# Kernel optimization log

Measured on AMD Instinct MI355X. Metric: run time of the kernel, lower is better.

The kernel has to match this reference:

```python
import jax, jax.numpy as jnp
import numpy as np

N0, N1, N2 = 1200000, 120000, 12000  # nodes per hop (outermost -> seeds)
E0, E1 = 1200000, 120000
IN_C, HID_C, OUT_C = 256, 256, 64


def setup_inputs() -> dict:
    key = jax.random.key(0)
    ks = jax.random.split(key, 10)
    s_in, s_hid = 1.0 / np.sqrt(IN_C), 1.0 / np.sqrt(HID_C)
    return {
        "x": jax.random.normal(ks[0], (N0, IN_C), dtype=jnp.float32),
        "src0": jax.random.randint(ks[1], (E0,), 0, N0, dtype=jnp.int64),
        "dst0": jax.random.randint(ks[2], (E0,), 0, N1, dtype=jnp.int64),
        "src1": jax.random.randint(ks[3], (E1,), 0, N1, dtype=jnp.int64),
        "dst1": jax.random.randint(ks[4], (E1,), 0, N2, dtype=jnp.int64),
        "Wl0": jax.random.normal(ks[5], (HID_C, IN_C), dtype=jnp.float32) * s_in,
        "b0": jnp.zeros((HID_C,), dtype=jnp.float32),
        "Wr0": jax.random.normal(ks[6], (HID_C, IN_C), dtype=jnp.float32) * s_in,
        "Wl1": jax.random.normal(ks[7], (OUT_C, HID_C), dtype=jnp.float32) * s_hid,
        "b1": jnp.zeros((OUT_C,), dtype=jnp.float32),
        "Wr1": jax.random.normal(ks[8], (OUT_C, HID_C), dtype=jnp.float32) * s_hid,
    }


def _sage_conv(x_src, x_tgt, src, dst, Wl, b, Wr, n_tgt):
    # gather neighbor (source) features, mean-scatter onto targets
    msg = x_src[src]                                          # [E, C]
    agg = jax.ops.segment_sum(msg, dst, num_segments=n_tgt)   # [n_tgt, C]
    cnt = jax.ops.segment_sum(jnp.ones((dst.shape[0],), x_src.dtype), dst,
                              num_segments=n_tgt)
    agg = agg / jnp.maximum(cnt, 1.0)[:, None]
    return agg @ Wl.T + b + x_tgt @ Wr.T


def reference(x, src0, dst0, src1, dst1, Wl0, b0, Wr0, Wl1, b1, Wr1):
    # layer 0 (eval mode: dropout is identity)
    h = _sage_conv(x, x[:N1], src0, dst0, Wl0, b0, Wr0, N1)
    h = jax.nn.relu(h)
    # layer 1
    out = _sage_conv(h, h[:N2], src1, dst1, Wl1, b1, Wr1, N2)
    return jax.nn.log_softmax(out, axis=-1)
```

## Files before the change

### kernel.cpp

```cpp
#include <hip/hip_runtime.h>
#include <stdint.h>

#define N0c 1200000
#define N1c 120000
#define N2c 12000
#define E0c 1200000
#define E1c 120000
#define NB0 118
#define NB1 12
#define N1pad 120064
#define N2pad 12032
#define ROWB 80
#define ROWU 40
#define HB 5157
#define WCB 768

typedef short short8 __attribute__((ext_vector_type(8)));
typedef float f32x4 __attribute__((ext_vector_type(4)));
typedef unsigned short u16;

__device__ __forceinline__ u16 f2bf(float f) {
    union { float f; unsigned u; } v; v.f = f;
    unsigned r = v.u + 0x7FFFu + ((v.u >> 16) & 1u);
    return (u16)(r >> 16);
}

__device__ __forceinline__ void gload16(const char* g, char* l) {
    __builtin_amdgcn_global_load_lds(
        (const __attribute__((address_space(1))) void*)g,
        (__attribute__((address_space(3))) void*)l, 16, 0, 0);
}

__global__ void k_hist(const int* __restrict__ dst0, const int* __restrict__ dst1,
                       int* __restrict__ c0, int* __restrict__ c1,
                       u16* __restrict__ Bt0, const float* __restrict__ Wl0,
                       const float* __restrict__ Wr0, u16* __restrict__ Bt1,
                       const float* __restrict__ Wl1, const float* __restrict__ Wr1) {
    if (blockIdx.x < HB) {
        int i = blockIdx.x * 256 + threadIdx.x;
        int part = blockIdx.x & 7;
        if (i < E0c) atomicAdd(&c0[part * N1c + dst0[i]], 1);
        else if (i < E0c + E1c) atomicAdd(&c1[part * N2c + dst1[i - E0c]], 1);
    } else {
        int i = (blockIdx.x - HB) * 256 + threadIdx.x;
        if (i < 256 * 512) {
            int c = i >> 9, k = i & 511;
            float v = (k < 256) ? Wl0[c * 256 + k] : Wr0[c * 256 + (k - 256)];
            Bt0[((size_t)(k >> 5) * 256 + c) * ROWU + (k & 31)] = f2bf(v);
        } else {
            int j = i - 256 * 512;
            int c = j >> 9, k = j & 511;
            float v = 0.f;
            if (c < 64) v = (k < 256) ? Wl1[c * 256 + k] : Wr1[c * 256 + (k - 256)];
            Bt1[j] = f2bf(v);
        }
    }
}

__global__ void k_scanA(const int* __restrict__ c0, const int* __restrict__ c1,
                        int* __restrict__ partials) {
    __shared__ int sh[256];
    int hop = blockIdx.x >= NB0;
    int blk = hop ? blockIdx.x - NB0 : blockIdx.x;
    const int* c = hop ? c1 : c0;
    int n = hop ? N2c : N1c;
    int d0 = blk * 1024 + threadIdx.x * 4;
    int tsum = 0;
#pragma unroll
    for (int j = 0; j < 4; ++j) {
        int d = d0 + j;
        if (d < n)
#pragma unroll
            for (int k = 0; k < 8; ++k) tsum += c[k * n + d];
    }
    sh[threadIdx.x] = tsum;
    __syncthreads();
    for (int ofs = 128; ofs > 0; ofs >>= 1) {
        if (threadIdx.x < ofs) sh[threadIdx.x] += sh[threadIdx.x + ofs];
        __syncthreads();
    }
    if (threadIdx.x == 0) partials[blockIdx.x] = sh[0];
}

__global__ void k_scanB(int* __restrict__ partials, int* __restrict__ rs0,
                        int* __restrict__ rs1) {
    __shared__ int sh[256];
    int tid = threadIdx.x;
    int v0 = tid < NB0 ? partials[tid] : 0;
    sh[tid] = v0; __syncthreads();
    for (int ofs = 1; ofs < 256; ofs <<= 1) {
        int t = tid >= ofs ? sh[tid - ofs] : 0;
        __syncthreads();
        sh[tid] += t;
        __syncthreads();
    }
    if (tid < NB0) partials[tid] = sh[tid] - v0;
    __syncthreads();
    int v1 = tid < NB1 ? partials[NB0 + tid] : 0;
    sh[tid] = v1; __syncthreads();
    for (int ofs = 1; ofs < 256; ofs <<= 1) {
        int t = tid >= ofs ? sh[tid - ofs] : 0;
        __syncthreads();
        sh[tid] += t;
        __syncthreads();
    }
    if (tid < NB1) partials[NB0 + tid] = sh[tid] - v1;
    if (tid == 0) { rs0[N1c] = E0c; rs1[N2c] = E1c; }
}

__global__ void k_scanC(const int* __restrict__ c0, const int* __restrict__ c1,
                        const int* __restrict__ partials, int* __restrict__ rs0,
                        int* __restrict__ rs1, int* __restrict__ bs0,
                        int* __restrict__ bs1) {
    __shared__ int sh[256];
    int hop = blockIdx.x >= NB0;
    int blk = hop ? blockIdx.x - NB0 : blockIdx.x;
    const int* c = hop ? c1 : c0;
    int* rs = hop ? rs1 : rs0;
    int* bs = hop ? bs1 : bs0;
    int n = hop ? N2c : N1c;
    int tid = threadIdx.x;
    int d0 = blk * 1024 + tid * 4;
    int cv[4][8];
    int tsum = 0;
#pragma unroll
    for (int j = 0; j < 4; ++j)
#pragma unroll
        for (int k = 0; k < 8; ++k) {
            int d = d0 + j;
            int v = (d < n) ? c[k * n + d] : 0;
            cv[j][k] = v; tsum += v;
        }
    sh[tid] = tsum; __syncthreads();
    for (int ofs = 1; ofs < 256; ofs <<= 1) {
        int t = tid >= ofs ? sh[tid - ofs] : 0;
        __syncthreads();
        sh[tid] += t;
        __syncthreads();
    }
    int run = partials[blockIdx.x] + sh[tid] - tsum;
#pragma unroll
    for (int j = 0; j < 4; ++j) {
        int d = d0 + j;
        if (d < n) {
            rs[d] = run;
#pragma unroll
            for (int k = 0; k < 8; ++k) { bs[k * n + d] = run; run += cv[j][k]; }
        }
    }
}

__global__ void k_scat(const int* __restrict__ src0, const int* __restrict__ dst0,
                       const int* __restrict__ src1, const int* __restrict__ dst1,
                       int* __restrict__ c0, int* __restrict__ c1,
                       const int* __restrict__ bs0, const int* __restrict__ bs1,
                       int* __restrict__ eidx0, int* __restrict__ eidx1) {
    int i = blockIdx.x * 256 + threadIdx.x;
    int part = blockIdx.x & 7;
    if (i < E0c) {
        int d = dst0[i];
        int off = atomicSub(&c0[part * N1c + d], 1) - 1;
        eidx0[bs0[part * N1c + d] + off] = src0[i];
    } else if (i < E0c + E1c) {
        int j = i - E0c;
        int d = dst1[j];
        int off = atomicSub(&c1[part * N2c + d], 1) - 1;
        eidx1[bs1[part * N2c + d] + off] = src1[j];
    }
}

__global__ void k_agg0(const float* __restrict__ x, const int* __restrict__ eidx,
                       const int* __restrict__ rs, u16* __restrict__ A, int ntgt) {
    int w = (int)((blockIdx.x * blockDim.x + threadIdx.x) >> 6);
    int lane = threadIdx.x & 63;
    if (w >= ntgt) return;
    int s = rs[w], e = rs[w + 1];
    float a0 = 0.f, a1 = 0.f, a2 = 0.f, a3 = 0.f;
    int i = s;
    for (; i + 8 <= e; i += 8) {
        f32x4 v[8];
#pragma unroll
        for (int u = 0; u < 8; ++u)
            v[u] = __builtin_nontemporal_load(
                ((const f32x4*)(x + (long)eidx[i + u] * 256)) + lane);
#pragma unroll
        for (int u = 0; u < 8; ++u) {
            a0 += v[u][0]; a1 += v[u][1]; a2 += v[u][2]; a3 += v[u][3];
        }
    }
    for (; i + 2 <= e; i += 2) {
        f32x4 v0 = __builtin_nontemporal_load(
            ((const f32x4*)(x + (long)eidx[i] * 256)) + lane);
        f32x4 v1 = __builtin_nontemporal_load(
            ((const f32x4*)(x + (long)eidx[i + 1] * 256)) + lane);
        a0 += v0[0] + v1[0]; a1 += v0[1] + v1[1];
        a2 += v0[2] + v1[2]; a3 += v0[3] + v1[3];
    }
    if (i < e) {
        f32x4 v = __builtin_nontemporal_load(
            ((const f32x4*)(x + (long)eidx[i] * 256)) + lane);
        a0 += v[0]; a1 += v[1]; a2 += v[2]; a3 += v[3];
    }
    int c = e - s; if (c < 1) c = 1;
    float sc = 1.f / (float)c;
    int kt = lane >> 3;
    int cu = (lane & 7) * 4;
    ushort4 oa;
    oa.x = f2bf(a0 * sc); oa.y = f2bf(a1 * sc); oa.z = f2bf(a2 * sc); oa.w = f2bf(a3 * sc);
    *(ushort4*)(A + ((size_t)kt * N1pad + w) * ROWU + cu) = oa;
}

__global__ void k_agg1(const u16* __restrict__ hsrc, const int* __restrict__ eidx,
                       const int* __restrict__ rs, u16* __restrict__ A, int ntgt) {
    int w = (int)((blockIdx.x * blockDim.x + threadIdx.x) >> 6);
    int lane = threadIdx.x & 63;
    if (w >= ntgt) return;
    int s = rs[w], e = rs[w + 1];
    float a0 = 0.f, a1 = 0.f, a2 = 0.f, a3 = 0.f;
    auto acc4 = [&](ushort4 v) {
        union { unsigned u; float f; } c0, c1, c2, c3;
        c0.u = (unsigned)v.x << 16; c1.u = (unsigned)v.y << 16;
        c2.u = (unsigned)v.z << 16; c3.u = (unsigned)v.w << 16;
        a0 += c0.f; a1 += c1.f; a2 += c2.f; a3 += c3.f;
    };
    int i = s;
    for (; i + 4 <= e; i += 4) {
        ushort4 v0 = ((const ushort4*)(hsrc + (long)eidx[i] * 256))[lane];
        ushort4 v1 = ((const ushort4*)(hsrc + (long)eidx[i + 1] * 256))[lane];
        ushort4 v2 = ((const ushort4*)(hsrc + (long)eidx[i + 2] * 256))[lane];
        ushort4 v3 = ((const ushort4*)(hsrc + (long)eidx[i + 3] * 256))[lane];
        acc4(v0); acc4(v1); acc4(v2); acc4(v3);
    }
    for (; i < e; ++i) {
        ushort4 v = ((const ushort4*)(hsrc + (long)eidx[i] * 256))[lane];
        acc4(v);
    }
    int c = e - s; if (c < 1) c = 1;
    float sc = 1.f / (float)c;
    ushort4 o;
    o.x = f2bf(a0 * sc); o.y = f2bf(a1 * sc); o.z = f2bf(a2 * sc); o.w = f2bf(a3 * sc);
    *(ushort4*)(A + (long)w * 512 + lane * 4) = o;
    ushort4 sv = ((const ushort4*)(hsrc + (long)w * 256))[lane];
    *(ushort4*)(A + (long)w * 512 + 256 + lane * 4) = sv;
}

__global__ __launch_bounds__(512)
void k_gemm0(const u16* __restrict__ A0, const float* __restrict__ x,
             const u16* __restrict__ Bt, const float* __restrict__ bias,
             u16* __restrict__ outp) {
    __shared__ int4 Lbuf[2 * 30720 / 16];
    char* L = (char*)Lbuf;
    const int tid = threadIdx.x;
    const int lane = tid & 63, wid = tid >> 6;
    const int wm = wid >> 2, wn = wid & 3;
    const long m0 = (long)blockIdx.x * 128;

    f32x4 acc[4][4];
#pragma unroll
    for (int i = 0; i < 4; ++i)
#pragma unroll
        for (int j = 0; j < 4; ++j) acc[i][j] = (f32x4){0.f, 0.f, 0.f, 0.f};

    const char* Abase = (const char*)A0 + m0 * ROWB;
    const char* Bbase = (const char*)Bt;
    const int srow = tid >> 2, scq = tid & 3;

    auto stage = [&](int buf, int kt) {
        char* lb = L + buf * 30720;
        const char* gb = Bbase + (size_t)kt * (256 * ROWB);
        if (kt < 8) {
            const char* ga = Abase + (size_t)kt * ((size_t)N1pad * ROWB);
#pragma unroll
            for (int c0 = 0; c0 < 4; ++c0) {
                int c = wid + c0 * 8;
                if (c < 30) {
                    const char* g = (c < 10) ? (ga + c * 1024) : (gb + (c - 10) * 1024);
                    gload16(g + lane * 16, lb + c * 1024);
                }
            }
        } else {
#pragma unroll
            for (int c0 = 0; c0 < 3; ++c0) {
                int c = wid + c0 * 8;
                if (c < 20) gload16(gb + c * 1024 + lane * 16, lb + 10240 + c * 1024);
            }
            const f32x4* p =
                (const f32x4*)(x + (m0 + srow) * 256 + (kt - 8) * 32 + scq * 8);
            f32x4 v0 = p[0], v1 = p[1];
            ushort4 h0, h1;
            h0.x = f2bf(v0[0]); h0.y = f2bf(v0[1]); h0.z = f2bf(v0[2]); h0.w = f2bf(v0[3]);
            h1.x = f2bf(v1[0]); h1.y = f2bf(v1[1]); h1.z = f2bf(v1[2]); h1.w = f2bf(v1[3]);
            ushort4* d = (ushort4*)(lb + srow * ROWB + scq * 16);
            d[0] = h0; d[1] = h1;
        }
    };

    stage(0, 0);
    const int rr = lane & 15, gg = lane >> 4;
    for (int ks = 0; ks < 16; ++ks) {
        int cur = ks & 1;
        __syncthreads();
        if (ks + 1 < 16) stage(cur ^ 1, ks + 1);
        const char* lb = L + cur * 30720;
        short8 af[4], bv[4];
#pragma unroll
        for (int f = 0; f < 4; ++f) {
            af[f] = *(const short8*)(lb + (wm * 64 + f * 16 + rr) * ROWB + gg * 16);
            bv[f] = *(const short8*)(lb + 10240 + (wn * 64 + f * 16 + rr) * ROWB + gg * 16);
        }
#pragma unroll
        for (int i = 0; i < 4; ++i)
#pragma unroll
            for (int j = 0; j < 4; ++j)
                acc[i][j] =
                    __builtin_amdgcn_mfma_f32_16x16x32_bf16(af[i], bv[j], acc[i][j], 0, 0, 0);
    }

#pragma unroll
    for (int j = 0; j < 4; ++j) {
        int col = wn * 64 + j * 16 + rr;
        float bvl = bias[col];
#pragma unroll
        for (int i = 0; i < 4; ++i) {
            long row = m0 + wm * 64 + i * 16 + gg * 4;
#pragma unroll
            for (int q = 0; q < 4; ++q) {
                long r = row + q;
                if (r < N1c) {
                    float v = acc[i][j][q] + bvl;
                    v = v > 0.f ? v : 0.f;
                    outp[r * 256 + col] = f2bf(v);
                }
            }
        }
    }
}

__global__ __launch_bounds__(256)
void k_gemm1(const u16* __restrict__ A, const u16* __restrict__ Bt,
             const float* __restrict__ bias, float* __restrict__ outp) {
    __shared__ u16 As[128 * 40];
    __shared__ u16 Bs[128 * 40];
    const int tid = threadIdx.x;
    const int lane = tid & 63, wid = tid >> 6;
    const int wm = wid >> 1, wn = wid & 1;
    const long m0 = (long)blockIdx.x * 128;
    const int sar = tid >> 1, sac = (tid & 1) * 16;

    f32x4 acc[4][4];
#pragma unroll
    for (int i = 0; i < 4; ++i)
#pragma unroll
        for (int j = 0; j < 4; ++j) acc[i][j] = (f32x4){0.f, 0.f, 0.f, 0.f};

    int4 ra[2]; int4 rb[2];
    auto load_tile = [&](int ks) {
        int k0 = ks * 32;
        const int4* p = (const int4*)(A + (m0 + sar) * 512 + k0 + sac);
        ra[0] = p[0]; ra[1] = p[1];
        const int4* q = (const int4*)(Bt + (long)sar * 512 + k0 + sac);
        rb[0] = q[0]; rb[1] = q[1];
    };
    auto write_tile = [&]() {
        int4* da = (int4*)(As + sar * 40 + sac);
        da[0] = ra[0]; da[1] = ra[1];
        int4* db = (int4*)(Bs + sar * 40 + sac);
        db[0] = rb[0]; db[1] = rb[1];
    };

    load_tile(0);
    for (int ks = 0; ks < 16; ++ks) {
        __syncthreads();
        write_tile();
        __syncthreads();
        if (ks + 1 < 16) load_tile(ks + 1);
        short8 af[4], bv[4];
        const int rr = lane & 15, gg = lane >> 4;
#pragma unroll
        for (int f = 0; f < 4; ++f) {
            af[f] = *(const short8*)(As + (wm * 64 + f * 16 + rr) * 40 + gg * 8);
            bv[f] = *(const short8*)(Bs + (wn * 64 + f * 16 + rr) * 40 + gg * 8);
        }
#pragma unroll
        for (int i = 0; i < 4; ++i)
#pragma unroll
            for (int j = 0; j < 4; ++j)
                acc[i][j] =
                    __builtin_amdgcn_mfma_f32_16x16x32_bf16(af[i], bv[j], acc[i][j], 0, 0, 0);
    }

    const int rr = lane & 15, gg = lane >> 4;
    if (wn == 0) {
#pragma unroll
        for (int i = 0; i < 4; ++i) {
#pragma unroll
            for (int q = 0; q < 4; ++q) {
                long r = m0 + wm * 64 + i * 16 + gg * 4 + q;
                float v[4];
#pragma unroll
                for (int j = 0; j < 4; ++j) v[j] = acc[i][j][q] + bias[j * 16 + rr];
                float mx = fmaxf(fmaxf(v[0], v[1]), fmaxf(v[2], v[3]));
#pragma unroll
                for (int m = 1; m < 16; m <<= 1) mx = fmaxf(mx, __shfl_xor(mx, m, 16));
                float se = __expf(v[0] - mx) + __expf(v[1] - mx) +
                           __expf(v[2] - mx) + __expf(v[3] - mx);
#pragma unroll
                for (int m = 1; m < 16; m <<= 1) se += __shfl_xor(se, m, 16);
                float ln = __logf(se);
                if (r < N2c) {
#pragma unroll
                    for (int j = 0; j < 4; ++j)
                        outp[r * 64 + j * 16 + rr] = v[j] - mx - ln;
                }
            }
        }
    }
}

extern "C" void kernel_launch(void* const* d_in, const int* in_sizes, int n_in,
                              void* d_out, int out_size, void* d_ws, size_t ws_size,
                              hipStream_t stream) {
    const float* x   = (const float*)d_in[0];
    const int* src0  = (const int*)d_in[1];
    const int* dst0  = (const int*)d_in[2];
    const int* src1  = (const int*)d_in[3];
    const int* dst1  = (const int*)d_in[4];
    const float* Wl0 = (const float*)d_in[5];
    const float* b0  = (const float*)d_in[6];
    const float* Wr0 = (const float*)d_in[7];
    const float* Wl1 = (const float*)d_in[8];
    const float* b1  = (const float*)d_in[9];
    const float* Wr1 = (const float*)d_in[10];

    char* base = (char*)d_ws;
    size_t off = 0;
    auto alloc = [&](size_t bytes) -> void* {
        off = (off + 255) & ~(size_t)255;
        void* p = base + off;
        off += bytes;
        return p;
    };
    int* c0       = (int*)alloc((size_t)8 * N1c * 4);
    int* c1       = (int*)alloc((size_t)8 * N2c * 4);
    int* bs0      = (int*)alloc((size_t)8 * N1c * 4);
    int* bs1      = (int*)alloc((size_t)8 * N2c * 4);
    int* rs0      = (int*)alloc((size_t)(N1c + 1) * 4);
    int* rs1      = (int*)alloc((size_t)(N2c + 1) * 4);
    int* partials = (int*)alloc((size_t)(NB0 + NB1) * 4);
    int* eidx0    = (int*)alloc((size_t)E0c * 4);
    int* eidx1    = (int*)alloc((size_t)E1c * 4);
    u16* A0       = (u16*)alloc((size_t)8 * N1pad * ROWU * 2);
    u16* hbuf     = (u16*)alloc((size_t)N1pad * 256 * 2);
    u16* A1       = (u16*)alloc((size_t)N2pad * 512 * 2);
    u16* Bt0      = (u16*)alloc((size_t)16 * 256 * ROWU * 2);
    u16* Bt1      = (u16*)alloc((size_t)128 * 512 * 2);

    (void)hipMemsetAsync(c0, 0, (size_t)8 * (N1c + N2c) * 4, stream);

    k_hist<<<HB + WCB, 256, 0, stream>>>(dst0, dst1, c0, c1,
                                         Bt0, Wl0, Wr0, Bt1, Wl1, Wr1);
    k_scanA<<<NB0 + NB1, 256, 0, stream>>>(c0, c1, partials);
    k_scanB<<<1, 256, 0, stream>>>(partials, rs0, rs1);
    k_scanC<<<NB0 + NB1, 256, 0, stream>>>(c0, c1, partials, rs0, rs1, bs0, bs1);
    k_scat<<<HB, 256, 0, stream>>>(src0, dst0, src1, dst1,
                                   c0, c1, bs0, bs1, eidx0, eidx1);

    k_agg0<<<(N1c + 3) / 4, 256, 0, stream>>>(x, eidx0, rs0, A0, N1c);
    k_gemm0<<<N1pad / 128, 512, 0, stream>>>(A0, x, Bt0, b0, hbuf);

    k_agg1<<<(N2c + 3) / 4, 256, 0, stream>>>(hbuf, eidx1, rs1, A1, N2c);
    k_gemm1<<<N2pad / 128, 256, 0, stream>>>(A1, Bt1, b1, (float*)d_out);
}
```

Before: 533.0 us.

## Pack scatter base and count into u64, drop nontemporal gathers, split GEMM staging

The scatter kernel now does a single 64-bit atomic on a packed (base offset, count) word instead of an atomicSub plus a separate load of the base array. The aggregation gathers switch from nontemporal loads to normal cached loads, so repeated source rows can hit in cache. In the layer-0 GEMM, staging of the fp32 x tile is split into a global load issued before the MFMAs and a bf16 convert-and-LDS-write after them, so load latency overlaps compute. Costs are a wider packed scratch array and extra registers held across the MFMA loop.

```diff
diff --git a/kernel.cpp b/kernel.cpp
--- a/kernel.cpp
+++ b/kernel.cpp
@@ -18,6 +18,7 @@
 typedef short short8 __attribute__((ext_vector_type(8)));
 typedef float f32x4 __attribute__((ext_vector_type(4)));
 typedef unsigned short u16;
+typedef unsigned long long u64;
 
 __device__ __forceinline__ u16 f2bf(float f) {
     union { float f; unsigned u; } v; v.f = f;
@@ -110,14 +111,14 @@
 
 __global__ void k_scanC(const int* __restrict__ c0, const int* __restrict__ c1,
                         const int* __restrict__ partials, int* __restrict__ rs0,
-                        int* __restrict__ rs1, int* __restrict__ bs0,
-                        int* __restrict__ bs1) {
+                        int* __restrict__ rs1, u64* __restrict__ pk0,
+                        u64* __restrict__ pk1) {
     __shared__ int sh[256];
     int hop = blockIdx.x >= NB0;
     int blk = hop ? blockIdx.x - NB0 : blockIdx.x;
     const int* c = hop ? c1 : c0;
     int* rs = hop ? rs1 : rs0;
-    int* bs = hop ? bs1 : bs0;
+    u64* pk = hop ? pk1 : pk0;
     int n = hop ? N2c : N1c;
     int tid = threadIdx.x;
     int d0 = blk * 1024 + tid * 4;
@@ -145,27 +146,29 @@
         if (d < n) {
             rs[d] = run;
 #pragma unroll
-            for (int k = 0; k < 8; ++k) { bs[k * n + d] = run; run += cv[j][k]; }
+            for (int k = 0; k < 8; ++k) {
+                pk[(size_t)k * n + d] = ((u64)(unsigned)run << 32) | (unsigned)cv[j][k];
+                run += cv[j][k];
+            }
         }
     }
 }
 
 __global__ void k_scat(const int* __restrict__ src0, const int* __restrict__ dst0,
                        const int* __restrict__ src1, const int* __restrict__ dst1,
-                       int* __restrict__ c0, int* __restrict__ c1,
-                       const int* __restrict__ bs0, const int* __restrict__ bs1,
+                       u64* __restrict__ pk0, u64* __restrict__ pk1,
                        int* __restrict__ eidx0, int* __restrict__ eidx1) {
     int i = blockIdx.x * 256 + threadIdx.x;
     int part = blockIdx.x & 7;
     if (i < E0c) {
         int d = dst0[i];
-        int off = atomicSub(&c0[part * N1c + d], 1) - 1;
-        eidx0[bs0[part * N1c + d] + off] = src0[i];
+        u64 old = atomicAdd(&pk0[(size_t)part * N1c + d], (u64)-1);
+        eidx0[(int)(old >> 32) + (int)(old & 0xffffffffu) - 1] = src0[i];
     } else if (i < E0c + E1c) {
         int j = i - E0c;
         int d = dst1[j];
-        int off = atomicSub(&c1[part * N2c + d], 1) - 1;
-        eidx1[bs1[part * N2c + d] + off] = src1[j];
+        u64 old = atomicAdd(&pk1[(size_t)part * N2c + d], (u64)-1);
+        eidx1[(int)(old >> 32) + (int)(old & 0xffffffffu) - 1] = src1[j];
     }
 }
 
@@ -181,24 +184,20 @@
         f32x4 v[8];
 #pragma unroll
         for (int u = 0; u < 8; ++u)
-            v[u] = __builtin_nontemporal_load(
-                ((const f32x4*)(x + (long)eidx[i + u] * 256)) + lane);
+            v[u] = ((const f32x4*)(x + (long)eidx[i + u] * 256))[lane];
 #pragma unroll
         for (int u = 0; u < 8; ++u) {
             a0 += v[u][0]; a1 += v[u][1]; a2 += v[u][2]; a3 += v[u][3];
         }
     }
     for (; i + 2 <= e; i += 2) {
-        f32x4 v0 = __builtin_nontemporal_load(
-            ((const f32x4*)(x + (long)eidx[i] * 256)) + lane);
-        f32x4 v1 = __builtin_nontemporal_load(
-            ((const f32x4*)(x + (long)eidx[i + 1] * 256)) + lane);
+        f32x4 v0 = ((const f32x4*)(x + (long)eidx[i] * 256))[lane];
+        f32x4 v1 = ((const f32x4*)(x + (long)eidx[i + 1] * 256))[lane];
         a0 += v0[0] + v1[0]; a1 += v0[1] + v1[1];
         a2 += v0[2] + v1[2]; a3 += v0[3] + v1[3];
     }
     if (i < e) {
-        f32x4 v = __builtin_nontemporal_load(
-            ((const f32x4*)(x + (long)eidx[i] * 256)) + lane);
+        f32x4 v = ((const f32x4*)(x + (long)eidx[i] * 256))[lane];
         a0 += v[0]; a1 += v[1]; a2 += v[2]; a3 += v[3];
     }
     int c = e - s; if (c < 1) c = 1;
@@ -264,8 +263,9 @@
     const char* Abase = (const char*)A0 + m0 * ROWB;
     const char* Bbase = (const char*)Bt;
     const int srow = tid >> 2, scq = tid & 3;
-
-    auto stage = [&](int buf, int kt) {
+    f32x4 xv0, xv1;
+
+    auto stage_load = [&](int buf, int kt) {
         char* lb = L + buf * 30720;
         const char* gb = Bbase + (size_t)kt * (256 * ROWB);
         if (kt < 8) {
@@ -286,21 +286,28 @@
             }
             const f32x4* p =
                 (const f32x4*)(x + (m0 + srow) * 256 + (kt - 8) * 32 + scq * 8);
-            f32x4 v0 = p[0], v1 = p[1];
+            xv0 = p[0]; xv1 = p[1];
+        }
+    };
+    auto stage_write = [&](int buf, int kt) {
+        if (kt >= 8) {
+            char* lb = L + buf * 30720;
             ushort4 h0, h1;
-            h0.x = f2bf(v0[0]); h0.y = f2bf(v0[1]); h0.z = f2bf(v0[2]); h0.w = f2bf(v0[3]);
-            h1.x = f2bf(v1[0]); h1.y = f2bf(v1[1]); h1.z = f2bf(v1[2]); h1.w = f2bf(v1[3]);
+            h0.x = f2bf(xv0[0]); h0.y = f2bf(xv0[1]);
+            h0.z = f2bf(xv0[2]); h0.w = f2bf(xv0[3]);
+            h1.x = f2bf(xv1[0]); h1.y = f2bf(xv1[1]);
+            h1.z = f2bf(xv1[2]); h1.w = f2bf(xv1[3]);
             ushort4* d = (ushort4*)(lb + srow * ROWB + scq * 16);
             d[0] = h0; d[1] = h1;
         }
     };
 
-    stage(0, 0);
+    stage_load(0, 0);
     const int rr = lane & 15, gg = lane >> 4;
     for (int ks = 0; ks < 16; ++ks) {
         int cur = ks & 1;
         __syncthreads();
-        if (ks + 1 < 16) stage(cur ^ 1, ks + 1);
+        if (ks + 1 < 16) stage_load(cur ^ 1, ks + 1);
         const char* lb = L + cur * 30720;
         short8 af[4], bv[4];
 #pragma unroll
@@ -314,6 +321,7 @@
             for (int j = 0; j < 4; ++j)
                 acc[i][j] =
                     __builtin_amdgcn_mfma_f32_16x16x32_bf16(af[i], bv[j], acc[i][j], 0, 0, 0);
+        if (ks + 1 < 16) stage_write(cur ^ 1, ks + 1);
     }
 
 #pragma unroll
@@ -442,8 +450,8 @@
     };
     int* c0       = (int*)alloc((size_t)8 * N1c * 4);
     int* c1       = (int*)alloc((size_t)8 * N2c * 4);
-    int* bs0      = (int*)alloc((size_t)8 * N1c * 4);
-    int* bs1      = (int*)alloc((size_t)8 * N2c * 4);
+    u64* pk0      = (u64*)alloc((size_t)8 * N1c * 8);
+    u64* pk1      = (u64*)alloc((size_t)8 * N2c * 8);
     int* rs0      = (int*)alloc((size_t)(N1c + 1) * 4);
     int* rs1      = (int*)alloc((size_t)(N2c + 1) * 4);
     int* partials = (int*)alloc((size_t)(NB0 + NB1) * 4);
@@ -461,9 +469,9 @@
                                          Bt0, Wl0, Wr0, Bt1, Wl1, Wr1);
     k_scanA<<<NB0 + NB1, 256, 0, stream>>>(c0, c1, partials);
     k_scanB<<<1, 256, 0, stream>>>(partials, rs0, rs1);
-    k_scanC<<<NB0 + NB1, 256, 0, stream>>>(c0, c1, partials, rs0, rs1, bs0, bs1);
+    k_scanC<<<NB0 + NB1, 256, 0, stream>>>(c0, c1, partials, rs0, rs1, pk0, pk1);
     k_scat<<<HB, 256, 0, stream>>>(src0, dst0, src1, dst1,
-                                   c0, c1, bs0, bs1, eidx0, eidx1);
+                                   pk0, pk1, eidx0, eidx1);
 
     k_agg0<<<(N1c + 3) / 4, 256, 0, stream>>>(x, eidx0, rs0, A0, N1c);
     k_gemm0<<<N1pad / 128, 512, 0, stream>>>(A0, x, Bt0, b0, hbuf);
```

Measured after the change: 582.4 us. +9.3%, slower.
